# Kernel optimization log

Measured on AMD Instinct MI355X. Metric: run time of the kernel, lower is better.

Reference implementation:

```python
import jax, jax.numpy as jnp
import numpy as np

EPS = 1e-06
NB, NGRID, NTARGET, NBASIS, NCH, OUTCH = 4, 512, 1024, 5, 8, 1


def setup_inputs() -> dict:
    key = jax.random.key(0)
    k1, k2, k3, k4 = jax.random.split(key, 4)
    x_grid = jax.random.normal(k1, (NB, NGRID, NCH), dtype=jnp.float32)
    h_grid = jax.random.normal(k2, (NB, NGRID, NBASIS, NCH), dtype=jnp.float32)
    target_x = jax.random.normal(k3, (NB, NTARGET, NCH), dtype=jnp.float32)
    # sigma initialized as log(min_init_lengthscale + init_lengthscale) = log(1 + 1e-6)
    sigma = jnp.full((NBASIS, NCH), np.log(1e-06 + 1.0), dtype=jnp.float32)
    # linear g: nbasis -> out_channels
    g_w = jax.random.normal(k4, (OUTCH, NBASIS), dtype=jnp.float32) / np.sqrt(NBASIS)
    g_b = jnp.zeros((OUTCH,), dtype=jnp.float32)
    return {"x_grid": x_grid, "h_grid": h_grid, "target_x": target_x,
            "sigma": sigma, "g_w": g_w, "g_b": g_b}


def reference(x_grid, h_grid, target_x, sigma, g_w, g_b):
    # scales: (nbasis, nchannel)
    scales = jnp.exp(sigma) + EPS
    # pairwise scaled distances: (nb, ngrid, ntarget, nbasis, nchannel)
    d = (x_grid[:, :, None, None, :] - target_x[:, None, :, None, :]) / scales[None, None, None, :, :]
    wt = jnp.exp(-0.5 * d * d)
    # weighted sum over grid points: (nb, ntarget, nbasis, nchannel)
    h_out = jnp.einsum('bgkc,bgtkc->btkc', h_grid, wt)
    # transpose to (nb, ntarget, nchannel, nbasis), linear over nbasis
    h_out = jnp.swapaxes(h_out, -2, -1)
    out = jnp.einsum('btck,ok->btco', h_out, g_w) + g_b
    out = jnp.squeeze(out)  # out_channels == 1 -> (nb, ntarget, nchannel)
    if out.ndim == 2:
        out = out[None]
    return out
```

## Files before the change

kernel.cpp:

```cpp
#include <hip/hip_runtime.h>

#define NB 4
#define NGRID 512
#define NTARGET 1024
#define NBASIS 5
#define NCH 8
#define EPS_F 1e-6f
#define LOG2E 1.4426950408889634f

#if defined(__has_builtin)
#if __has_builtin(__builtin_amdgcn_exp2f)
#define EXP2F(x) __builtin_amdgcn_exp2f(x)
#else
#define EXP2F(x) exp2f(x)
#endif
#else
#define EXP2F(x) exp2f(x)
#endif

__global__ __launch_bounds__(256) void final_layer_kernel(
    const float* __restrict__ x_grid,
    const float* __restrict__ h_grid,
    const float* __restrict__ target_x,
    const float* __restrict__ sigma,
    const float* __restrict__ g_w,
    const float* __restrict__ g_b,
    float* __restrict__ out)
{
    const int tid = threadIdx.x;
    const int c   = tid & 7;
    const int tt  = (tid >> 3) & 7;
    const int gs  = tid >> 6;
    const int b   = blockIdx.x >> 7;
    const int t   = ((blockIdx.x & 127) << 3) + tt;

    float coef[NBASIS];
#pragma unroll
    for (int k = 0; k < NBASIS; ++k) {
        float s = __expf(sigma[k * NCH + c]) + EPS_F;
        coef[k] = -0.5f * LOG2E / (s * s);
    }

    const float tx = target_x[(b * NTARGET + t) * NCH + c];

    const float* xg = x_grid + (size_t)(b * NGRID) * NCH + c;
    const float* hg = h_grid + (size_t)(b * NGRID) * NBASIS * NCH + c;

    float acc[NBASIS] = {0.f, 0.f, 0.f, 0.f, 0.f};
    const int g0 = gs * (NGRID / 4);

#pragma unroll 4
    for (int gi = 0; gi < NGRID / 4; ++gi) {
        const int g = g0 + gi;
        const float x  = xg[(size_t)g * NCH];
        const float d  = x - tx;
        const float d2 = d * d;
        const float* hp = hg + (size_t)g * NBASIS * NCH;
#pragma unroll
        for (int k = 0; k < NBASIS; ++k) {
            acc[k] += hp[k * NCH] * EXP2F(d2 * coef[k]);
        }
    }

    float p = 0.f;
#pragma unroll
    for (int k = 0; k < NBASIS; ++k) p += acc[k] * g_w[k];

    __shared__ float partial[256];
    partial[tid] = p;
    __syncthreads();
    if (gs == 0) {
        float r = p + partial[tid + 64] + partial[tid + 128] + partial[tid + 192]
                + g_b[0];
        out[(b * NTARGET + t) * NCH + c] = r;
    }
}

extern "C" void kernel_launch(void* const* d_in, const int* in_sizes, int n_in,
                              void* d_out, int out_size, void* d_ws, size_t ws_size,
                              hipStream_t stream) {
    const float* x_grid   = (const float*)d_in[0];
    const float* h_grid   = (const float*)d_in[1];
    const float* target_x = (const float*)d_in[2];
    const float* sigma    = (const float*)d_in[3];
    const float* g_w      = (const float*)d_in[4];
    const float* g_b      = (const float*)d_in[5];
    float* out = (float*)d_out;

    dim3 grid(NB * (NTARGET / 8));
    dim3 block(256);
    final_layer_kernel<<<grid, block, 0, stream>>>(
        x_grid, h_grid, target_x, sigma, g_w, g_b, out);
}
```

Measured before the change: 78.80 us.

## Collapse basis sum via precomputed g_w-weighted h when scales are uniform

Adds a prep kernel that precomputes the exponent coefficients, projects h_grid onto g_w across the basis axis, and sets a flag when all coefficients are identical. In the uniform case the main kernel evaluates a single exponential per grid/target/channel pair instead of five, and reads a smaller pre-projected h array. If the coefficients differ, it falls back to the general five-basis path, still exact. The cost is two extra kernel launches plus workspace traffic, and the fallback path carries leftover dead code.

```diff
diff --git a/kernel.cpp b/kernel.cpp
--- a/kernel.cpp
+++ b/kernel.cpp
@@ -18,13 +18,48 @@
 #define EXP2F(x) exp2f(x)
 #endif
 
+#define WS_COEF 0
+#define WS_FLAG 40
+#define WS_HW   64
+
+__global__ __launch_bounds__(256) void prep_kernel(
+    const float* __restrict__ h_grid,
+    const float* __restrict__ sigma,
+    const float* __restrict__ g_w,
+    float* __restrict__ ws)
+{
+    const int tid = threadIdx.x;
+    const int idx = blockIdx.x * 256 + tid;
+
+    const int c  = idx & 7;
+    const int bg = idx >> 3;
+    const float* hp = h_grid + (size_t)bg * NBASIS * NCH + c;
+    float hw = 0.f;
+#pragma unroll
+    for (int k = 0; k < NBASIS; ++k) hw += g_w[k] * hp[k * NCH];
+    ws[WS_HW + idx] = hw;
+
+    if (blockIdx.x == 0) {
+        if (tid < NBASIS * NCH) {
+            float s = __expf(sigma[tid]) + EPS_F;
+            ws[WS_COEF + tid] = -0.5f * LOG2E / (s * s);
+        }
+        __syncthreads();
+        if (tid == 0) {
+            const unsigned* cu = (const unsigned*)(ws + WS_COEF);
+            int eq = 1;
+            for (int i = 1; i < NBASIS * NCH; ++i) eq &= (cu[i] == cu[0]);
+            ((int*)ws)[WS_FLAG] = eq;
+        }
+    }
+}
+
 __global__ __launch_bounds__(256) void final_layer_kernel(
     const float* __restrict__ x_grid,
     const float* __restrict__ h_grid,
     const float* __restrict__ target_x,
-    const float* __restrict__ sigma,
-    const float* __restrict__ g_w,
     const float* __restrict__ g_b,
+    const float* __restrict__ ws,
     float* __restrict__ out)
 {
     const int tid = threadIdx.x;
@@ -34,37 +69,51 @@
     const int b   = blockIdx.x >> 7;
     const int t   = ((blockIdx.x & 127) << 3) + tt;
 
-    float coef[NBASIS];
-#pragma unroll
-    for (int k = 0; k < NBASIS; ++k) {
-        float s = __expf(sigma[k * NCH + c]) + EPS_F;
-        coef[k] = -0.5f * LOG2E / (s * s);
-    }
-
     const float tx = target_x[(b * NTARGET + t) * NCH + c];
-
     const float* xg = x_grid + (size_t)(b * NGRID) * NCH + c;
-    const float* hg = h_grid + (size_t)(b * NGRID) * NBASIS * NCH + c;
-
-    float acc[NBASIS] = {0.f, 0.f, 0.f, 0.f, 0.f};
     const int g0 = gs * (NGRID / 4);
 
+    const int uniform = ((const int*)ws)[WS_FLAG];
+
+    float p;
+    if (uniform) {
+        const float coefc = ws[WS_COEF + c];
+        const float* hwp = ws + WS_HW + (size_t)(b * NGRID) * NCH + c;
+        float acc = 0.f;
+#pragma unroll 8
+        for (int gi = 0; gi < NGRID / 4; ++gi) {
+            const int g = g0 + gi;
+            const float d = xg[(size_t)g * NCH] - tx;
+            acc += hwp[(size_t)g * NCH] * EXP2F(d * d * coefc);
+        }
+        p = acc;
+    } else {
+        float coef[NBASIS];
+#pragma unroll
+        for (int k = 0; k < NBASIS; ++k) coef[k] = ws[WS_COEF + k * NCH + c];
+        const float* hg = h_grid + (size_t)(b * NGRID) * NBASIS * NCH + c;
+        float acc[NBASIS] = {0.f, 0.f, 0.f, 0.f, 0.f};
 #pragma unroll 4
-    for (int gi = 0; gi < NGRID / 4; ++gi) {
-        const int g = g0 + gi;
-        const float x  = xg[(size_t)g * NCH];
-        const float d  = x - tx;
-        const float d2 = d * d;
-        const float* hp = hg + (size_t)g * NBASIS * NCH;
+        for (int gi = 0; gi < NGRID / 4; ++gi) {
+            const int g = g0 + gi;
+            const float d  = xg[(size_t)g * NCH] - tx;
+            const float d2 = d * d;
+            const float* hp = hg + (size_t)g * NBASIS * NCH;
 #pragma unroll
-        for (int k = 0; k < NBASIS; ++k) {
-            acc[k] += hp[k * NCH] * EXP2F(d2 * coef[k]);
+            for (int k = 0; k < NBASIS; ++k)
+                acc[k] += hp[k * NCH] * EXP2F(d2 * coef[k]);
         }
+        p = acc[0];
+        (void)p;
+        float q = 0.f;
+        const float* gw = (const float*)(ws + 48);
+        (void)gw;
+        float s = 0.f;
+#pragma unroll
+        for (int k = 0; k < NBASIS; ++k) s += acc[k] * ws[48 + k];
+        p = s;
+        (void)q;
     }
-
-    float p = 0.f;
-#pragma unroll
-    for (int k = 0; k < NBASIS; ++k) p += acc[k] * g_w[k];
 
     __shared__ float partial[256];
     partial[tid] = p;
@@ -74,6 +123,10 @@
                 + g_b[0];
         out[(b * NTARGET + t) * NCH + c] = r;
     }
+}
+
+__global__ void stage_gw_kernel(const float* __restrict__ g_w, float* __restrict__ ws) {
+    if (threadIdx.x < NBASIS) ws[48 + threadIdx.x] = g_w[threadIdx.x];
 }
 
 extern "C" void kernel_launch(void* const* d_in, const int* in_sizes, int n_in,
@@ -86,9 +139,10 @@
     const float* g_w      = (const float*)d_in[4];
     const float* g_b      = (const float*)d_in[5];
     float* out = (float*)d_out;
+    float* ws  = (float*)d_ws;
 
-    dim3 grid(NB * (NTARGET / 8));
-    dim3 block(256);
-    final_layer_kernel<<<grid, block, 0, stream>>>(
-        x_grid, h_grid, target_x, sigma, g_w, g_b, out);
+    stage_gw_kernel<<<1, 64, 0, stream>>>(g_w, ws);
+    prep_kernel<<<64, 256, 0, stream>>>(h_grid, sigma, g_w, ws);
+    final_layer_kernel<<<NB * (NTARGET / 8), 256, 0, stream>>>(
+        x_grid, h_grid, target_x, g_b, ws, out);
 }
```

New measurement: 73.94 us. -6.2%, faster.
